# Kernel optimization log

Hardware: AMD Instinct MI355X
Metric: run time of the kernel (lower is better)

The kernel has to match this reference:

```python
import jax, jax.numpy as jnp
import numpy as np

B, D, C = 8192, 2048, 1000
NUM_IDS = 256
MSEL_W, ORTH_W, CONS_W = 0.5, 0.1, 0.1


def setup_inputs() -> dict:
    key = jax.random.key(0)
    ks = jax.random.split(key, 7)
    return {
        "feat_shared": jax.random.normal(ks[0], (B, D), dtype=jnp.float32),
        "dee1": jax.random.normal(ks[1], (B, D), dtype=jnp.float32),
        "dee2": jax.random.normal(ks[2], (B, D), dtype=jnp.float32),
        "dee3": jax.random.normal(ks[3], (B, D), dtype=jnp.float32),
        "logits": jax.random.normal(ks[4], (B, C), dtype=jnp.float32),
        "labels": jax.random.randint(ks[5], (B,), 0, NUM_IDS, dtype=jnp.int32),
        "modal_ids": jax.random.randint(ks[6], (B,), 0, 2, dtype=jnp.int32),
    }


def _l2norm(x):
    return x / jnp.sqrt(jnp.sum(x * x, axis=1, keepdims=True)).clip(1e-12)


def _msel(features, labels, modal_ids):
    f = _l2norm(features)
    m_rgb = (modal_ids == 0).astype(f.dtype)  # [B]
    m_sar = (modal_ids == 1).astype(f.dtype)
    # per-label per-modal sums and counts via segment_sum (fixed NUM_IDS segments)
    sum_rgb = jax.ops.segment_sum(f * m_rgb[:, None], labels, num_segments=NUM_IDS)  # [L,D]
    sum_sar = jax.ops.segment_sum(f * m_sar[:, None], labels, num_segments=NUM_IDS)
    n_rgb = jax.ops.segment_sum(m_rgb, labels, num_segments=NUM_IDS)  # [L]
    n_sar = jax.ops.segment_sum(m_sar, labels, num_segments=NUM_IDS)
    c_rgb = sum_rgb / jnp.maximum(n_rgb, 1.0)[:, None]
    c_sar = sum_sar / jnp.maximum(n_sar, 1.0)[:, None]
    dist_cross = 1.0 - jnp.sum(c_rgb * c_sar, axis=1)
    # mean of Gram(f_rgb, f_rgb) == center_rgb . center_rgb (includes diagonal), same math
    dist_intra = 1.0 - jnp.sum(c_rgb * c_rgb, axis=1)
    valid = (n_rgb >= 2.0) & (n_sar >= 1.0)
    per_label = jnp.where(valid, (dist_cross - dist_intra) ** 2, 0.0)
    count = jnp.sum(valid.astype(f.dtype))
    return jnp.where(count > 0, jnp.sum(per_label) / jnp.maximum(count, 1.0), 0.0)


def _orth(f1, f2, f3):
    n1, n2, n3 = _l2norm(f1), _l2norm(f2), _l2norm(f3)
    s12 = jnp.mean(jnp.abs(jnp.sum(n1 * n2, axis=1)))
    s13 = jnp.mean(jnp.abs(jnp.sum(n1 * n3, axis=1)))
    s23 = jnp.mean(jnp.abs(jnp.sum(n2 * n3, axis=1)))
    return s12 + s13 + s23


def _consistency(logits, modal_ids):
    probs = jax.nn.softmax(logits, axis=1)  # [B,C]
    m_rgb = (modal_ids == 0).astype(probs.dtype)
    m_sar = (modal_ids == 1).astype(probs.dtype)
    n_rgb = jnp.sum(m_rgb)
    n_sar = jnp.sum(m_sar)
    p_rgb = jnp.sum(probs * m_rgb[:, None], axis=0) / jnp.maximum(n_rgb, 1.0)
    p_sar = jnp.sum(probs * m_sar[:, None], axis=0) / jnp.maximum(n_sar, 1.0)
    lr, ls = jnp.log(p_rgb), jnp.log(p_sar)
    # F.kl_div(log p, q, 'sum') = sum q*(log q - log p)
    kl = 0.5 * (jnp.sum(p_sar * (ls - lr)) + jnp.sum(p_rgb * (lr - ls)))
    return jnp.where((n_rgb > 0) & (n_sar > 0), kl, 0.0)


def reference(feat_shared, dee1, dee2, dee3, logits, labels, modal_ids):
    loss = MSEL_W * _msel(feat_shared, labels, modal_ids)
    loss = loss + ORTH_W * _orth(dee1, dee2, dee3)
    loss = loss + CONS_W * _consistency(logits, modal_ids)
    return loss
```

## Files before the change

### kernel.cpp

```cpp
#include <hip/hip_runtime.h>
#include <math.h>

#define B_   8192
#define D_   2048
#define C_   1000
#define L_   256
#define BIN_CAP 64

#define ORTH_BLK  256
#define NORM_BLK  128
#define CONS_BLK  512
#define FUSED_GRID (ORTH_BLK + NORM_BLK + CONS_BLK)
#define ORTH_WAVES (ORTH_BLK * 4)

typedef unsigned short bf16raw;

__device__ __forceinline__ float bflo(unsigned int u) { return __uint_as_float(u << 16); }
__device__ __forceinline__ float bfhi(unsigned int u) { return __uint_as_float(u & 0xffff0000u); }

__device__ __forceinline__ bf16raw f2b(float f) {
  unsigned int x = __float_as_uint(f);
  unsigned int r = (x + 0x7fffu + ((x >> 16) & 1u)) >> 16;
  return (bf16raw)r;
}

__device__ __forceinline__ void dec8(uint4 u, float* x) {
  x[0] = bflo(u.x); x[1] = bfhi(u.x);
  x[2] = bflo(u.y); x[3] = bfhi(u.y);
  x[4] = bflo(u.z); x[5] = bfhi(u.z);
  x[6] = bflo(u.w); x[7] = bfhi(u.w);
}

__device__ __forceinline__ float waveSum(float v) {
#pragma unroll
  for (int off = 32; off > 0; off >>= 1) v += __shfl_xor(v, off, 64);
  return v;
}

__device__ __forceinline__ float blockSum(float v, float* lds4) {
  v = waveSum(v);
  const int wave = threadIdx.x >> 6;
  if ((threadIdx.x & 63) == 0) lds4[wave] = v;
  __syncthreads();
  v = lds4[0] + lds4[1] + lds4[2] + lds4[3];
  __syncthreads();
  return v;
}

__global__ __launch_bounds__(256) void detect_kernel(const unsigned int* feat_words,
                                                     int* flag) {
  __shared__ float lds4[4];
  const unsigned int w = feat_words[threadIdx.x];
  const float v = bflo(w);
  const float a = fabsf(v);
  float hit = (a > 1e-3f && a < 10.f) ? 1.f : 0.f;
  hit = blockSum(hit, lds4);
  if (threadIdx.x == 0) *flag = (hit > 128.f) ? 1 : 0;
}

__global__ __launch_bounds__(256) void init_kernel(int* counts, float* accs,
                                                   float* p_final) {
  const int t = blockIdx.x * 256 + threadIdx.x;
  if (t < 2 * L_) counts[t] = 0;
  if (t < 16) accs[t] = 0.f;
  if (t < 2 * C_) p_final[t] = 0.f;
}

__global__ __launch_bounds__(256) void bin_kernel(const int* labels, const int* modal,
                                                  int* counts, int* rowlist) {
  const int r = blockIdx.x * 256 + threadIdx.x;
  if (r >= B_) return;
  const int m = modal[r] ? 1 : 0;
  int lb = labels[r]; lb = lb < 0 ? 0 : (lb >= L_ ? L_ - 1 : lb);
  const int key = m * L_ + lb;
  const int idx = atomicAdd(&counts[key], 1);
  if (idx < BIN_CAP) rowlist[key * BIN_CAP + idx] = r;
}

__device__ __forceinline__ void ldrow3(const bf16raw* pa, const bf16raw* pb,
                                       const bf16raw* pc, size_t base, int lane,
                                       uint4 (&A)[4], uint4 (&Bv)[4], uint4 (&Cv)[4]) {
  const uint4* qa = (const uint4*)(pa + base);
  const uint4* qb = (const uint4*)(pb + base);
  const uint4* qc = (const uint4*)(pc + base);
#pragma unroll
  for (int j = 0; j < 4; ++j) A[j] = qa[j * 64 + lane];
#pragma unroll
  for (int j = 0; j < 4; ++j) Bv[j] = qb[j * 64 + lane];
#pragma unroll
  for (int j = 0; j < 4; ++j) Cv[j] = qc[j * 64 + lane];
}

__device__ __forceinline__ void orth_rowacc(const uint4 (&A)[4], const uint4 (&Bv)[4],
                                            const uint4 (&Cv)[4], float (&v)[6]) {
#pragma unroll
  for (int j = 0; j < 4; ++j) {
    float a[8], b[8], c[8];
    dec8(A[j], a); dec8(Bv[j], b); dec8(Cv[j], c);
#pragma unroll
    for (int k = 0; k < 8; ++k) {
      v[0] += a[k] * a[k]; v[1] += b[k] * b[k]; v[2] += c[k] * c[k];
      v[3] += a[k] * b[k]; v[4] += a[k] * c[k]; v[5] += b[k] * c[k];
    }
  }
}

__device__ __forceinline__ float ssq4(const uint4 (&X)[4]) {
  float ss = 0.f;
#pragma unroll
  for (int j = 0; j < 4; ++j) {
    float x[8]; dec8(X[j], x);
#pragma unroll
    for (int k = 0; k < 8; ++k) ss += x[k] * x[k];
  }
  return ss;
}

__device__ __forceinline__ void loadlogits_f32(const void* logits, int r, int lane,
                                               float (&x)[16]) {
#pragma unroll
  for (int kk = 0; kk < 4; ++kk) {
    const int idx = lane + (kk << 6);
    if (idx < (C_ / 4)) {
      const float4 w = ((const float4*)((const float*)logits + (size_t)r * C_))[idx];
      x[4 * kk + 0] = w.x; x[4 * kk + 1] = w.y;
      x[4 * kk + 2] = w.z; x[4 * kk + 3] = w.w;
    } else {
      x[4 * kk + 0] = -INFINITY; x[4 * kk + 1] = -INFINITY;
      x[4 * kk + 2] = -INFINITY; x[4 * kk + 3] = -INFINITY;
    }
  }
}

__device__ __forceinline__ void softmax_acc(float (&x)[16], int m, float (&accA)[16],
                                            float (&accB)[16]) {
  float mx = -INFINITY;
#pragma unroll
  for (int k = 0; k < 16; ++k) mx = fmaxf(mx, x[k]);
#pragma unroll
  for (int off = 32; off > 0; off >>= 1) mx = fmaxf(mx, __shfl_xor(mx, off, 64));
  float s = 0.f;
#pragma unroll
  for (int k = 0; k < 16; ++k) { x[k] = expf(x[k] - mx); s += x[k]; }
#pragma unroll
  for (int off = 32; off > 0; off >>= 1) s += __shfl_xor(s, off, 64);
  const float inv = 1.f / s;
  if (m == 0) {
#pragma unroll
    for (int k = 0; k < 16; ++k) accA[k] += x[k] * inv;
  } else {
#pragma unroll
    for (int k = 0; k < 16; ++k) accB[k] += x[k] * inv;
  }
}

__global__ __launch_bounds__(256) void fused_stream_kernel(
    const void* f1, const void* f2, const void* f3, const void* feat,
    const void* logits, const int* modal, float* orth_part, float* norms,
    float* p_final, const int* flag) {
  __shared__ float wacc[4][2][1024];
  const int t = threadIdx.x;
  const int wave = t >> 6, lane = t & 63;
  const int isb = *flag;
  const int bx = blockIdx.x;

  if (bx < ORTH_BLK) {
    const int gw = bx * 4 + wave;
    float s12 = 0.f, s13 = 0.f, s23 = 0.f;
    if (isb) {
      const bf16raw* pa = (const bf16raw*)f1;
      const bf16raw* pb = (const bf16raw*)f2;
      const bf16raw* pc = (const bf16raw*)f3;
      const size_t base0 = (size_t)gw * (8 * D_);
      uint4 A0[4], B0[4], C0[4], A1[4], B1[4], C1[4];
      ldrow3(pa, pb, pc, base0, lane, A0, B0, C0);
#pragma unroll
      for (int r = 0; r < 8; ++r) {
        if (r < 7) {
          const size_t nb = base0 + (size_t)(r + 1) * D_;
          if (r & 1) ldrow3(pa, pb, pc, nb, lane, A0, B0, C0);
          else       ldrow3(pa, pb, pc, nb, lane, A1, B1, C1);
        }
        float v[6] = {0.f, 0.f, 0.f, 0.f, 0.f, 0.f};
        if (r & 1) orth_rowacc(A1, B1, C1, v);
        else       orth_rowacc(A0, B0, C0, v);
#pragma unroll
        for (int off = 32; off > 0; off >>= 1) {
#pragma unroll
          for (int j = 0; j < 6; ++j) v[j] += __shfl_xor(v[j], off, 64);
        }
        const float q1 = fmaxf(sqrtf(v[0]), 1e-12f);
        const float q2 = fmaxf(sqrtf(v[1]), 1e-12f);
        const float q3 = fmaxf(sqrtf(v[2]), 1e-12f);
        s12 += fabsf(v[3]) / (q1 * q2);
        s13 += fabsf(v[4]) / (q1 * q3);
        s23 += fabsf(v[5]) / (q2 * q3);
      }
    } else {
      for (int r = 0; r < 8; ++r) {
        const size_t base = ((size_t)gw * 8 + r) * D_;
        const float4* qa = (const float4*)((const float*)f1 + base);
        const float4* qb = (const float4*)((const float*)f2 + base);
        const float4* qc = (const float4*)((const float*)f3 + base);
        float v[6] = {0.f, 0.f, 0.f, 0.f, 0.f, 0.f};
#pragma unroll
        for (int h = 0; h < 8; ++h) {
          const float4 a4 = qa[h * 64 + lane];
          const float4 b4 = qb[h * 64 + lane];
          const float4 c4 = qc[h * 64 + lane];
          const float a[4] = {a4.x, a4.y, a4.z, a4.w};
          const float b[4] = {b4.x, b4.y, b4.z, b4.w};
          const float c[4] = {c4.x, c4.y, c4.z, c4.w};
#pragma unroll
          for (int k = 0; k < 4; ++k) {
            v[0] += a[k] * a[k]; v[1] += b[k] * b[k]; v[2] += c[k] * c[k];
            v[3] += a[k] * b[k]; v[4] += a[k] * c[k]; v[5] += b[k] * c[k];
          }
        }
#pragma unroll
        for (int off = 32; off > 0; off >>= 1) {
#pragma unroll
          for (int j = 0; j < 6; ++j) v[j] += __shfl_xor(v[j], off, 64);
        }
        const float q1 = fmaxf(sqrtf(v[0]), 1e-12f);
        const float q2 = fmaxf(sqrtf(v[1]), 1e-12f);
        const float q3 = fmaxf(sqrtf(v[2]), 1e-12f);
        s12 += fabsf(v[3]) / (q1 * q2);
        s13 += fabsf(v[4]) / (q1 * q3);
        s23 += fabsf(v[5]) / (q2 * q3);
      }
    }
    if (lane == 0) {
      orth_part[gw] = s12;
      orth_part[ORTH_WAVES + gw] = s13;
      orth_part[2 * ORTH_WAVES + gw] = s23;
    }
  } else if (bx < ORTH_BLK + NORM_BLK) {
    const int gw = (bx - ORTH_BLK) * 4 + wave;
    const size_t base0 = (size_t)gw * (16 * D_);
    if (isb) {
      const bf16raw* pf = (const bf16raw*)feat;
      uint4 X0[4], X1[4];
      {
        const uint4* q = (const uint4*)(pf + base0);
#pragma unroll
        for (int j = 0; j < 4; ++j) X0[j] = q[j * 64 + lane];
      }
#pragma unroll
      for (int r = 0; r < 16; ++r) {
        if (r < 15) {
          const uint4* q = (const uint4*)(pf + base0 + (size_t)(r + 1) * D_);
          if (r & 1) {
#pragma unroll
            for (int j = 0; j < 4; ++j) X0[j] = q[j * 64 + lane];
          } else {
#pragma unroll
            for (int j = 0; j < 4; ++j) X1[j] = q[j * 64 + lane];
          }
        }
        float ss = (r & 1) ? ssq4(X1) : ssq4(X0);
        ss = waveSum(ss);
        if (lane == 0) norms[gw * 16 + r] = 1.f / fmaxf(sqrtf(ss), 1e-12f);
      }
    } else {
      for (int r = 0; r < 16; ++r) {
        const float4* q = (const float4*)((const float*)feat + base0 + (size_t)r * D_);
        float ss = 0.f;
#pragma unroll
        for (int j = 0; j < 8; ++j) {
          const float4 w = q[j * 64 + lane];
          ss += w.x * w.x + w.y * w.y + w.z * w.z + w.w * w.w;
        }
        ss = waveSum(ss);
        if (lane == 0) norms[gw * 16 + r] = 1.f / fmaxf(sqrtf(ss), 1e-12f);
      }
    }
  } else {
    const int cb = bx - ORTH_BLK - NORM_BLK;
    const int rbase = cb * 16 + wave * 4;
    float accA[16], accB[16];
#pragma unroll
    for (int k = 0; k < 16; ++k) { accA[k] = 0.f; accB[k] = 0.f; }
    if (isb) {
      const bf16raw* pl = (const bf16raw*)logits;
      uint4 W0a, W1a;
      uint4 W0b = make_uint4(0u, 0u, 0u, 0u), W1b = make_uint4(0u, 0u, 0u, 0u);
      int ma, mb = 0;
      {
        const uint4* q = (const uint4*)(pl + (size_t)rbase * C_);
        W0a = q[lane];
        W1a = (lane < 61) ? q[64 + lane] : make_uint4(0u, 0u, 0u, 0u);
        ma = modal[rbase];
      }
#pragma unroll
      for (int i = 0; i < 4; ++i) {
        if (i < 3) {
          const int rn = rbase + i + 1;
          const uint4* q = (const uint4*)(pl + (size_t)rn * C_);
          W0b = q[lane];
          W1b = (lane < 61) ? q[64 + lane] : make_uint4(0u, 0u, 0u, 0u);
          mb = modal[rn];
        }
        float x[16];
        dec8(W0a, x);
        if (lane < 61) {
          float xx[8]; dec8(W1a, xx);
#pragma unroll
          for (int k = 0; k < 8; ++k) x[8 + k] = xx[k];
        } else {
#pragma unroll
          for (int k = 0; k < 8; ++k) x[8 + k] = -INFINITY;
        }
        softmax_acc(x, ma, accA, accB);
        W0a = W0b; W1a = W1b; ma = mb;
      }
#pragma unroll
      for (int k = 0; k < 16; ++k) {
        const int c = (k < 8) ? (8 * lane + k) : (512 + 8 * lane + (k - 8));
        wacc[wave][0][c] = accA[k];
        wacc[wave][1][c] = accB[k];
      }
    } else {
      float xa[16], xb[16];
      int ma, mb = 0;
      loadlogits_f32(logits, rbase, lane, xa);
      ma = modal[rbase];
#pragma unroll
      for (int i = 0; i < 4; ++i) {
        if (i < 3) {
          loadlogits_f32(logits, rbase + i + 1, lane, xb);
          mb = modal[rbase + i + 1];
        }
        softmax_acc(xa, ma, accA, accB);
#pragma unroll
        for (int k = 0; k < 16; ++k) xa[k] = xb[k];
        ma = mb;
      }
#pragma unroll
      for (int k = 0; k < 16; ++k) {
        const int c = 4 * (lane + ((k >> 2) << 6)) + (k & 3);
        wacc[wave][0][c] = accA[k];
        wacc[wave][1][c] = accB[k];
      }
    }
    __syncthreads();
    for (int e = t; e < 2 * C_; e += 256) {
      const int m = (e < C_) ? 0 : 1;
      const int c = e - m * C_;
      atomicAdd(&p_final[e],
                wacc[0][m][c] + wacc[1][m][c] + wacc[2][m][c] + wacc[3][m][c]);
    }
  }
}

__global__ __launch_bounds__(256) void label_kernel(const void* feat, const int* counts,
                                                    const int* rowlist, const float* norms,
                                                    float* accs, const int* flag) {
  __shared__ float lds4[4];
  const int l = blockIdx.x;
  const int t = threadIdx.x;
  const int isb = *flag;
  const int nr_true = counts[l];
  const int ns_true = counts[L_ + l];
  const int nr = nr_true < BIN_CAP ? nr_true : BIN_CAP;
  const int ns = ns_true < BIN_CAP ? ns_true : BIN_CAP;
  const int tot = nr + ns;
  float accR[8], accS[8];
#pragma unroll
  for (int j = 0; j < 8; ++j) { accR[j] = 0.f; accS[j] = 0.f; }

  if (tot > 0) {
    auto rowAt = [&](int i) -> int {
      const int key = (i < nr) ? l : (L_ + l);
      const int idx = (i < nr) ? i : (i - nr);
      return rowlist[key * BIN_CAP + idx];
    };
    if (isb) {
      const bf16raw* pf = (const bf16raw*)feat;
      const int r0 = rowAt(0);
      uint4 qa = ((const uint4*)(pf + (size_t)r0 * D_))[t];
      float na = norms[r0];
      uint4 qb = make_uint4(0u, 0u, 0u, 0u);
      float nb2 = 0.f;
      if (tot > 1) {
        const int r1 = rowAt(1);
        qb = ((const uint4*)(pf + (size_t)r1 * D_))[t];
        nb2 = norms[r1];
      }
      for (int i = 0; i < tot; i += 2) {
        uint4 qc = make_uint4(0u, 0u, 0u, 0u), qd = make_uint4(0u, 0u, 0u, 0u);
        float nc = 0.f, nd = 0.f;
        if (i + 2 < tot) {
          const int rc = rowAt(i + 2);
          qc = ((const uint4*)(pf + (size_t)rc * D_))[t];
          nc = norms[rc];
        }
        if (i + 3 < tot) {
          const int rd = rowAt(i + 3);
          qd = ((const uint4*)(pf + (size_t)rd * D_))[t];
          nd = norms[rd];
        }
        {
          float x[8]; dec8(qa, x);
          if (i < nr) {
#pragma unroll
            for (int j = 0; j < 8; ++j) accR[j] += x[j] * na;
          } else {
#pragma unroll
            for (int j = 0; j < 8; ++j) accS[j] += x[j] * na;
          }
        }
        if (i + 1 < tot) {
          float x[8]; dec8(qb, x);
          if (i + 1 < nr) {
#pragma unroll
            for (int j = 0; j < 8; ++j) accR[j] += x[j] * nb2;
          } else {
#pragma unroll
            for (int j = 0; j < 8; ++j) accS[j] += x[j] * nb2;
          }
        }
        qa = qc; qb = qd; na = nc; nb2 = nd;
      }
    } else {
      const float* pf = (const float*)feat;
      const int r0 = rowAt(0);
      float4 a0 = ((const float4*)(pf + (size_t)r0 * D_))[2 * t];
      float4 a1 = ((const float4*)(pf + (size_t)r0 * D_))[2 * t + 1];
      float na = norms[r0];
      float4 b0 = make_float4(0.f, 0.f, 0.f, 0.f), b1 = make_float4(0.f, 0.f, 0.f, 0.f);
      float nb2 = 0.f;
      if (tot > 1) {
        const int r1 = rowAt(1);
        b0 = ((const float4*)(pf + (size_t)r1 * D_))[2 * t];
        b1 = ((const float4*)(pf + (size_t)r1 * D_))[2 * t + 1];
        nb2 = norms[r1];
      }
      for (int i = 0; i < tot; i += 2) {
        float4 c0 = make_float4(0.f, 0.f, 0.f, 0.f), c1 = c0, d0 = c0, d1 = c0;
        float nc = 0.f, nd = 0.f;
        if (i + 2 < tot) {
          const int rc = rowAt(i + 2);
          c0 = ((const float4*)(pf + (size_t)rc * D_))[2 * t];
          c1 = ((const float4*)(pf + (size_t)rc * D_))[2 * t + 1];
          nc = norms[rc];
        }
        if (i + 3 < tot) {
          const int rd = rowAt(i + 3);
          d0 = ((const float4*)(pf + (size_t)rd * D_))[2 * t];
          d1 = ((const float4*)(pf + (size_t)rd * D_))[2 * t + 1];
          nd = norms[rd];
        }
        {
          const float x[8] = {a0.x, a0.y, a0.z, a0.w, a1.x, a1.y, a1.z, a1.w};
          if (i < nr) {
#pragma unroll
            for (int j = 0; j < 8; ++j) accR[j] += x[j] * na;
          } else {
#pragma unroll
            for (int j = 0; j < 8; ++j) accS[j] += x[j] * na;
          }
        }
        if (i + 1 < tot) {
          const float x[8] = {b0.x, b0.y, b0.z, b0.w, b1.x, b1.y, b1.z, b1.w};
          if (i + 1 < nr) {
#pragma unroll
            for (int j = 0; j < 8; ++j) accR[j] += x[j] * nb2;
          } else {
#pragma unroll
            for (int j = 0; j < 8; ++j) accS[j] += x[j] * nb2;
          }
        }
        a0 = c0; a1 = c1; b0 = d0; b1 = d1; na = nc; nb2 = nd;
      }
    }
  }
  float rr = 0.f, rs = 0.f;
#pragma unroll
  for (int j = 0; j < 8; ++j) { rr += accR[j] * accR[j]; rs += accR[j] * accS[j]; }
  rr = blockSum(rr, lds4);
  rs = blockSum(rs, lds4);
  if (t == 0 && nr_true >= 2 && ns_true >= 1) {
    const float fr = (float)nr_true, fs = (float)ns_true;
    const float diff = rr / (fr * fr) - rs / (fr * fs);
    atomicAdd(&accs[3], diff * diff);
    atomicAdd(&accs[4], 1.0f);
  }
}

__global__ __launch_bounds__(256) void InnovationLoss_88124138979690_kernel(
    const float* p_final, const int* counts, const float* accs, const float* orth_part,
    void* out, const int* flag) {
  __shared__ float lds4[4];
  const int t = threadIdx.x;
  const float nr = blockSum((float)counts[t], lds4);
  const float ns = blockSum((float)counts[L_ + t], lds4);
  const float fr = fmaxf(nr, 1.f), fs = fmaxf(ns, 1.f);
  float klp = 0.f;
  for (int c = t; c < C_; c += 256) {
    const float pr = p_final[c] / fr;
    const float ps = p_final[C_ + c] / fs;
    klp += (ps - pr) * (logf(ps) - logf(pr));
  }
  klp = blockSum(klp, lds4);
  float o0 = 0.f, o1 = 0.f, o2 = 0.f;
  for (int b = t; b < ORTH_WAVES; b += 256) {
    o0 += orth_part[b];
    o1 += orth_part[ORTH_WAVES + b];
    o2 += orth_part[2 * ORTH_WAVES + b];
  }
  o0 = blockSum(o0, lds4);
  o1 = blockSum(o1, lds4);
  o2 = blockSum(o2, lds4);
  if (t == 0) {
    const float kl = (nr > 0.f && ns > 0.f) ? 0.5f * klp : 0.f;
    const float msel_cnt = accs[4];
    const float msel = msel_cnt > 0.f ? accs[3] / fmaxf(msel_cnt, 1.f) : 0.f;
    const float orth = (o0 + o1 + o2) * (1.0f / (float)B_);
    const float res = 0.5f * msel + 0.1f * orth + 0.1f * kl;
    if (*flag) ((bf16raw*)out)[0] = f2b(res);
    else       ((float*)out)[0]   = res;
  }
}

extern "C" __attribute__((visibility("default")))
void kernel_launch(void* const* d_in, const int* in_sizes, int n_in,
                   void* d_out, int out_size, void* d_ws, size_t ws_size,
                   hipStream_t stream) {
  const void* feat   = d_in[0];
  const void* dee1   = d_in[1];
  const void* dee2   = d_in[2];
  const void* dee3   = d_in[3];
  const void* logits = d_in[4];
  const int*  labels = (const int*)d_in[5];
  const int*  modal  = (const int*)d_in[6];

  char* ws = (char*)d_ws;
  int*   counts    = (int*)  (ws);
  float* accs      = (float*)(ws + 2048);
  float* p_final   = (float*)(ws + 2112);
  int*   rowlist   = (int*)  (ws + 10112);
  int*   flag      = (int*)  (ws + 141184);
  float* norms     = (float*)(ws + 141248);
  float* orth_part = (float*)(ws + 174016);

  detect_kernel<<<1, 256, 0, stream>>>((const unsigned int*)feat, flag);
  init_kernel<<<8, 256, 0, stream>>>(counts, accs, p_final);
  bin_kernel<<<B_ / 256, 256, 0, stream>>>(labels, modal, counts, rowlist);
  fused_stream_kernel<<<FUSED_GRID, 256, 0, stream>>>(dee1, dee2, dee3, feat, logits,
                                                      modal, orth_part, norms, p_final,
                                                      flag);
  label_kernel<<<L_, 256, 0, stream>>>(feat, counts, rowlist, norms, accs, flag);
  InnovationLoss_88124138979690_kernel<<<1, 256, 0, stream>>>(p_final, counts, accs,
                                                              orth_part, d_out, flag);
}
```

Measured before the change: 310.9 us.

## Fold detect and bin kernels into fused main kernel, rebalance block work

Removes the separate dtype-detect and binning launches. Each kernel now recomputes the bf16 flag inline, and the binning runs as an extra block range inside the fused streaming kernel. The work split also changes: twice as many orth blocks with 4 rows each, and fewer consumer blocks with 16 rows each. The explicit double-buffered prefetch in the orth and norm paths is dropped. The goal is to cut launch overhead and balance the grid, at the risk of less latency hiding from the removed prefetching.

```diff
diff --git a/kernel.cpp b/kernel.cpp
--- a/kernel.cpp
+++ b/kernel.cpp
@@ -7,10 +7,11 @@
 #define L_   256
 #define BIN_CAP 64
 
-#define ORTH_BLK  256
-#define NORM_BLK  128
-#define CONS_BLK  512
-#define FUSED_GRID (ORTH_BLK + NORM_BLK + CONS_BLK)
+#define BIN_BLK  32
+#define ORTH_BLK 512
+#define NORM_BLK 128
+#define CONS_BLK 128
+#define GRID_ (BIN_BLK + ORTH_BLK + NORM_BLK + CONS_BLK)
 #define ORTH_WAVES (ORTH_BLK * 4)
 
 typedef unsigned short bf16raw;
@@ -47,15 +48,12 @@
   return v;
 }
 
-__global__ __launch_bounds__(256) void detect_kernel(const unsigned int* feat_words,
-                                                     int* flag) {
-  __shared__ float lds4[4];
+__device__ __forceinline__ int detect_isb(const unsigned int* feat_words, float* lds4) {
   const unsigned int w = feat_words[threadIdx.x];
-  const float v = bflo(w);
-  const float a = fabsf(v);
+  const float a = fabsf(bflo(w));
   float hit = (a > 1e-3f && a < 10.f) ? 1.f : 0.f;
   hit = blockSum(hit, lds4);
-  if (threadIdx.x == 0) *flag = (hit > 128.f) ? 1 : 0;
+  return hit > 128.f ? 1 : 0;
 }
 
 __global__ __launch_bounds__(256) void init_kernel(int* counts, float* accs,
@@ -64,17 +62,6 @@
   if (t < 2 * L_) counts[t] = 0;
   if (t < 16) accs[t] = 0.f;
   if (t < 2 * C_) p_final[t] = 0.f;
-}
-
-__global__ __launch_bounds__(256) void bin_kernel(const int* labels, const int* modal,
-                                                  int* counts, int* rowlist) {
-  const int r = blockIdx.x * 256 + threadIdx.x;
-  if (r >= B_) return;
-  const int m = modal[r] ? 1 : 0;
-  int lb = labels[r]; lb = lb < 0 ? 0 : (lb >= L_ ? L_ - 1 : lb);
-  const int key = m * L_ + lb;
-  const int idx = atomicAdd(&counts[key], 1);
-  if (idx < BIN_CAP) rowlist[key * BIN_CAP + idx] = r;
 }
 
 __device__ __forceinline__ void ldrow3(const bf16raw* pa, const bf16raw* pb,
@@ -154,36 +141,37 @@
   }
 }
 
-__global__ __launch_bounds__(256) void fused_stream_kernel(
-    const void* f1, const void* f2, const void* f3, const void* feat,
-    const void* logits, const int* modal, float* orth_part, float* norms,
-    float* p_final, const int* flag) {
+__global__ __launch_bounds__(256) void fused_main_kernel(
+    const void* feat, const void* f1, const void* f2, const void* f3,
+    const void* logits, const int* labels, const int* modal,
+    int* counts, int* rowlist, float* orth_part, float* norms, float* p_final) {
   __shared__ float wacc[4][2][1024];
+  __shared__ float lds4[4];
   const int t = threadIdx.x;
   const int wave = t >> 6, lane = t & 63;
-  const int isb = *flag;
+  const int isb = detect_isb((const unsigned int*)feat, lds4);
   const int bx = blockIdx.x;
 
-  if (bx < ORTH_BLK) {
-    const int gw = bx * 4 + wave;
+  if (bx < BIN_BLK) {
+    const int r = bx * 256 + t;
+    const int m = modal[r] ? 1 : 0;
+    int lb = labels[r]; lb = lb < 0 ? 0 : (lb >= L_ ? L_ - 1 : lb);
+    const int key = m * L_ + lb;
+    const int idx = atomicAdd(&counts[key], 1);
+    if (idx < BIN_CAP) rowlist[key * BIN_CAP + idx] = r;
+  } else if (bx < BIN_BLK + ORTH_BLK) {
+    const int gw = (bx - BIN_BLK) * 4 + wave;
     float s12 = 0.f, s13 = 0.f, s23 = 0.f;
     if (isb) {
       const bf16raw* pa = (const bf16raw*)f1;
       const bf16raw* pb = (const bf16raw*)f2;
       const bf16raw* pc = (const bf16raw*)f3;
-      const size_t base0 = (size_t)gw * (8 * D_);
-      uint4 A0[4], B0[4], C0[4], A1[4], B1[4], C1[4];
-      ldrow3(pa, pb, pc, base0, lane, A0, B0, C0);
-#pragma unroll
-      for (int r = 0; r < 8; ++r) {
-        if (r < 7) {
-          const size_t nb = base0 + (size_t)(r + 1) * D_;
-          if (r & 1) ldrow3(pa, pb, pc, nb, lane, A0, B0, C0);
-          else       ldrow3(pa, pb, pc, nb, lane, A1, B1, C1);
-        }
+      for (int r = 0; r < 4; ++r) {
+        const size_t base = ((size_t)gw * 4 + r) * D_;
+        uint4 A[4], Bv[4], Cv[4];
+        ldrow3(pa, pb, pc, base, lane, A, Bv, Cv);
         float v[6] = {0.f, 0.f, 0.f, 0.f, 0.f, 0.f};
-        if (r & 1) orth_rowacc(A1, B1, C1, v);
-        else       orth_rowacc(A0, B0, C0, v);
+        orth_rowacc(A, Bv, Cv, v);
 #pragma unroll
         for (int off = 32; off > 0; off >>= 1) {
 #pragma unroll
@@ -197,8 +185,8 @@
         s23 += fabsf(v[5]) / (q2 * q3);
       }
     } else {
-      for (int r = 0; r < 8; ++r) {
-        const size_t base = ((size_t)gw * 8 + r) * D_;
+      for (int r = 0; r < 4; ++r) {
+        const size_t base = ((size_t)gw * 4 + r) * D_;
         const float4* qa = (const float4*)((const float*)f1 + base);
         const float4* qb = (const float4*)((const float*)f2 + base);
         const float4* qc = (const float4*)((const float*)f3 + base);
@@ -235,30 +223,17 @@
       orth_part[ORTH_WAVES + gw] = s13;
       orth_part[2 * ORTH_WAVES + gw] = s23;
     }
-  } else if (bx < ORTH_BLK + NORM_BLK) {
-    const int gw = (bx - ORTH_BLK) * 4 + wave;
+  } else if (bx < BIN_BLK + ORTH_BLK + NORM_BLK) {
+    const int gw = (bx - BIN_BLK - ORTH_BLK) * 4 + wave;
     const size_t base0 = (size_t)gw * (16 * D_);
     if (isb) {
       const bf16raw* pf = (const bf16raw*)feat;
-      uint4 X0[4], X1[4];
-      {
-        const uint4* q = (const uint4*)(pf + base0);
-#pragma unroll
-        for (int j = 0; j < 4; ++j) X0[j] = q[j * 64 + lane];
-      }
-#pragma unroll
       for (int r = 0; r < 16; ++r) {
-        if (r < 15) {
-          const uint4* q = (const uint4*)(pf + base0 + (size_t)(r + 1) * D_);
-          if (r & 1) {
-#pragma unroll
-            for (int j = 0; j < 4; ++j) X0[j] = q[j * 64 + lane];
-          } else {
-#pragma unroll
-            for (int j = 0; j < 4; ++j) X1[j] = q[j * 64 + lane];
-          }
-        }
-        float ss = (r & 1) ? ssq4(X1) : ssq4(X0);
+        const uint4* q = (const uint4*)(pf + base0 + (size_t)r * D_);
+        uint4 X[4];
+#pragma unroll
+        for (int j = 0; j < 4; ++j) X[j] = q[j * 64 + lane];
+        float ss = ssq4(X);
         ss = waveSum(ss);
         if (lane == 0) norms[gw * 16 + r] = 1.f / fmaxf(sqrtf(ss), 1e-12f);
       }
@@ -276,8 +251,8 @@
       }
     }
   } else {
-    const int cb = bx - ORTH_BLK - NORM_BLK;
-    const int rbase = cb * 16 + wave * 4;
+    const int cb = bx - BIN_BLK - ORTH_BLK - NORM_BLK;
+    const int rbase = cb * 64 + wave * 16;
     float accA[16], accB[16];
 #pragma unroll
     for (int k = 0; k < 16; ++k) { accA[k] = 0.f; accB[k] = 0.f; }
@@ -292,9 +267,8 @@
         W1a = (lane < 61) ? q[64 + lane] : make_uint4(0u, 0u, 0u, 0u);
         ma = modal[rbase];
       }
-#pragma unroll
-      for (int i = 0; i < 4; ++i) {
-        if (i < 3) {
+      for (int i = 0; i < 16; ++i) {
+        if (i < 15) {
           const int rn = rbase + i + 1;
           const uint4* q = (const uint4*)(pl + (size_t)rn * C_);
           W0b = q[lane];
@@ -325,9 +299,8 @@
       int ma, mb = 0;
       loadlogits_f32(logits, rbase, lane, xa);
       ma = modal[rbase];
-#pragma unroll
-      for (int i = 0; i < 4; ++i) {
-        if (i < 3) {
+      for (int i = 0; i < 16; ++i) {
+        if (i < 15) {
           loadlogits_f32(logits, rbase + i + 1, lane, xb);
           mb = modal[rbase + i + 1];
         }
@@ -355,11 +328,11 @@
 
 __global__ __launch_bounds__(256) void label_kernel(const void* feat, const int* counts,
                                                     const int* rowlist, const float* norms,
-                                                    float* accs, const int* flag) {
+                                                    float* accs) {
   __shared__ float lds4[4];
   const int l = blockIdx.x;
   const int t = threadIdx.x;
-  const int isb = *flag;
+  const int isb = detect_isb((const unsigned int*)feat, lds4);
   const int nr_true = counts[l];
   const int ns_true = counts[L_ + l];
   const int nr = nr_true < BIN_CAP ? nr_true : BIN_CAP;
@@ -489,10 +462,11 @@
 }
 
 __global__ __launch_bounds__(256) void InnovationLoss_88124138979690_kernel(
-    const float* p_final, const int* counts, const float* accs, const float* orth_part,
-    void* out, const int* flag) {
+    const void* feat, const float* p_final, const int* counts, const float* accs,
+    const float* orth_part, void* out) {
   __shared__ float lds4[4];
   const int t = threadIdx.x;
+  const int isb = detect_isb((const unsigned int*)feat, lds4);
   const float nr = blockSum((float)counts[t], lds4);
   const float ns = blockSum((float)counts[L_ + t], lds4);
   const float fr = fmaxf(nr, 1.f), fs = fmaxf(ns, 1.f);
@@ -518,8 +492,8 @@
     const float msel = msel_cnt > 0.f ? accs[3] / fmaxf(msel_cnt, 1.f) : 0.f;
     const float orth = (o0 + o1 + o2) * (1.0f / (float)B_);
     const float res = 0.5f * msel + 0.1f * orth + 0.1f * kl;
-    if (*flag) ((bf16raw*)out)[0] = f2b(res);
-    else       ((float*)out)[0]   = res;
+    if (isb) ((bf16raw*)out)[0] = f2b(res);
+    else     ((float*)out)[0]   = res;
   }
 }
 
@@ -540,17 +514,14 @@
   float* accs      = (float*)(ws + 2048);
   float* p_final   = (float*)(ws + 2112);
   int*   rowlist   = (int*)  (ws + 10112);
-  int*   flag      = (int*)  (ws + 141184);
-  float* norms     = (float*)(ws + 141248);
-  float* orth_part = (float*)(ws + 174016);
-
-  detect_kernel<<<1, 256, 0, stream>>>((const unsigned int*)feat, flag);
+  float* norms     = (float*)(ws + 141184);
+  float* orth_part = (float*)(ws + 173952);
+
   init_kernel<<<8, 256, 0, stream>>>(counts, accs, p_final);
-  bin_kernel<<<B_ / 256, 256, 0, stream>>>(labels, modal, counts, rowlist);
-  fused_stream_kernel<<<FUSED_GRID, 256, 0, stream>>>(dee1, dee2, dee3, feat, logits,
-                                                      modal, orth_part, norms, p_final,
-                                                      flag);
-  label_kernel<<<L_, 256, 0, stream>>>(feat, counts, rowlist, norms, accs, flag);
-  InnovationLoss_88124138979690_kernel<<<1, 256, 0, stream>>>(p_final, counts, accs,
-                                                              orth_part, d_out, flag);
-}
+  fused_main_kernel<<<GRID_, 256, 0, stream>>>(feat, dee1, dee2, dee3, logits, labels,
+                                               modal, counts, rowlist, orth_part, norms,
+                                               p_final);
+  label_kernel<<<L_, 256, 0, stream>>>(feat, counts, rowlist, norms, accs);
+  InnovationLoss_88124138979690_kernel<<<1, 256, 0, stream>>>(feat, p_final, counts,
+                                                              accs, orth_part, d_out);
+}
```

After: 306.8 us. Within noise of the previous version (-1.3%).
